# Kernel optimization log

Hardware: AMD Instinct MI355X
Metric: run time of the kernel (lower is better)

The kernel has to match this reference:

```python
import jax, jax.numpy as jnp
import numpy as np

N = 100000   # nodes
E = 800000   # edges (avg degree 8)
IN = 128     # in_dim
H = 128      # hidden_dim
L = 3        # num_layers
EPS = 1e-5   # torch LayerNorm default


def setup_inputs() -> dict:
    key = jax.random.key(0)
    ks = jax.random.split(key, 10)
    s = 0.05
    # DAG edge list: src < dst guarantees acyclicity and node N-1 is a sink.
    rng = np.random.default_rng(0)
    src = rng.integers(0, N - 1, size=E)
    dst = src + 1 + (rng.random(E) * (N - 1 - src)).astype(np.int64)
    return {
        "node_feats": jax.random.normal(ks[0], (N, IN), jnp.float32),
        "src": jnp.asarray(src, jnp.int32),
        "dst": jnp.asarray(dst, jnp.int32),
        "W_in": jax.random.normal(ks[1], (IN, H), jnp.float32) * s,
        "b_in": jnp.zeros((H,), jnp.float32),
        "Ws": jax.random.normal(ks[2], (L, H, H), jnp.float32) * s,
        "bs": jnp.zeros((L, H), jnp.float32),
        "Wn": jax.random.normal(ks[3], (L, H, H), jnp.float32) * s,
        "bn": jnp.zeros((L, H), jnp.float32),
        "Wg": jax.random.normal(ks[4], (L, 2 * H, H), jnp.float32) * s,
        "bg": jnp.zeros((L, H), jnp.float32),
        "gamma": jnp.ones((L, H), jnp.float32),
        "beta": jnp.zeros((L, H), jnp.float32),
        "W_att": jax.random.normal(ks[5], (H, H), jnp.float32) * s,
        "b_att": jnp.zeros((H,), jnp.float32),
        "W_score": jax.random.normal(ks[6], (H, 1), jnp.float32) * s,
        "b_score": jnp.zeros((1,), jnp.float32),
    }


def reference(node_feats, src, dst, W_in, b_in, Ws, bs, Wn, bn, Wg, bg,
              gamma, beta, W_att, b_att, W_score, b_score):
    n = node_feats.shape[0]
    ones_e = jnp.ones(src.shape, node_feats.dtype)
    indeg = jax.ops.segment_sum(ones_e, dst, num_segments=n)          # [N]
    has_pred = (indeg > 0).astype(node_feats.dtype)[:, None]          # [N,1]
    inv_deg = (1.0 / jnp.maximum(indeg, 1.0))[:, None]                # [N,1]
    outdeg = jax.ops.segment_sum(ones_e, src, num_segments=n)
    sink_mask = outdeg == 0                                           # [N]

    h = node_feats @ W_in + b_in                                      # [N,H]
    for i in range(Ws.shape[0]):
        hs = h @ Ws[i] + bs[i]
        # predecessor mean of layer-input h (no within-layer recurrence)
        neigh = jax.ops.segment_sum(h[src], dst, num_segments=n) * inv_deg
        hn = neigh @ Wn[i] + bn[i]
        m = hs + has_pred * hn  # nodes with no preds use m = hs only (bias too)
        gate = jax.nn.sigmoid(jnp.concatenate([h, m], axis=-1) @ Wg[i] + bg[i])
        v = gate * m + (1.0 - gate) * h
        mu = v.mean(-1, keepdims=True)
        var = ((v - mu) ** 2).mean(-1, keepdims=True)
        v = (v - mu) * jax.lax.rsqrt(var + EPS) * gamma[i] + beta[i]
        h = jax.nn.relu(v)

    # attention pooling over sink nodes only
    a = jnp.tanh(h @ W_att + b_att)
    scores = (a @ W_score)[:, 0] + b_score[0]
    scores = jnp.where(sink_mask, scores, -jnp.inf)
    w = jax.nn.softmax(scores, axis=0)  # zero weight on non-sinks
    graph_emb = (w[:, None] * h).sum(0)
    return h, graph_emb
```

## Files before the change

kernel.cpp:

```cpp
#include <hip/hip_runtime.h>
#include <cmath>

typedef unsigned short u16;
typedef unsigned int   u32;
typedef __attribute__((ext_vector_type(8))) short bf16x8;
typedef __attribute__((ext_vector_type(4))) float f32x4;
typedef __attribute__((ext_vector_type(4))) u32   u32x4;

__device__ __forceinline__ float bf2f(u16 u){
    union { u32 i; float f; } x; x.i = ((u32)u) << 16; return x.f;
}
__device__ __forceinline__ u16 f2bf(float f){
    union { float f; u32 i; } x; x.f = f;
    u32 r = x.i + 0x7fffu + ((x.i >> 16) & 1u);
    return (u16)(r >> 16);
}

__device__ __forceinline__ size_t frag_idx(int n, int k){
    int t = n >> 4, sl = n & 15, kk = k >> 5, g16 = (k >> 3) & 3, e = k & 7;
    return ((size_t)(t*4 + kk)*64 + g16*16 + sl)*8 + e;
}


__global__ void k_count(const int* __restrict__ src, const int* __restrict__ dst,
                        int* cnt, int* notsink, int* pos, int E){
    int e = blockIdx.x*256 + threadIdx.x;
    if (e < E){
        pos[e] = atomicAdd(&cnt[dst[e]], 1);
        notsink[src[e]] = 1;
    }
}

__global__ void k_scan1(const int* __restrict__ in, int* blocksum, int N){
    __shared__ int sh[256];
    int tid = threadIdx.x;
    int base = blockIdx.x*1024 + tid*4;
    int s = 0;
    for (int j=0;j<4;j++){ int i = base+j; s += (i < N) ? in[i] : 0; }
    sh[tid] = s; __syncthreads();
    for (int d=128; d>0; d>>=1){ if (tid < d) sh[tid] += sh[tid+d]; __syncthreads(); }
    if (tid == 0) blocksum[blockIdx.x] = sh[0];
}

__global__ void k_scan2(int* blocksum, int nb){
    if (threadIdx.x == 0){
        int run = 0;
        for (int i=0;i<nb;i++){ int v = blocksum[i]; blocksum[i] = run; run += v; }
    }
}

__global__ void k_scan3(const int* __restrict__ in, const int* __restrict__ blockoff,
                        int* out, float* inv_deg, float* haspred, int N){
    __shared__ int sh[256];
    int tid = threadIdx.x;
    int base = blockIdx.x*1024 + tid*4;
    int e[4]; int s = 0;
    for (int j=0;j<4;j++){ int i = base+j; e[j] = (i < N) ? in[i] : 0; s += e[j]; }
    sh[tid] = s; __syncthreads();
    for (int d=1; d<256; d<<=1){
        int t = (tid >= d) ? sh[tid-d] : 0;
        __syncthreads();
        sh[tid] += t;
        __syncthreads();
    }
    int excl = sh[tid] - s + blockoff[blockIdx.x];
    for (int j=0;j<4;j++){
        int i = base+j;
        if (i < N){
            out[i] = excl; excl += e[j];
            inv_deg[i] = 1.0f / (float)(e[j] > 1 ? e[j] : 1);
            haspred[i] = e[j] > 0 ? 1.0f : 0.0f;
        }
    }
}

__global__ void k_place(const int* __restrict__ src, const int* __restrict__ dst,
                        const int* __restrict__ row_ptr, const int* __restrict__ pos,
                        int* csr_src, int E){
    int e = blockIdx.x*256 + threadIdx.x;
    if (e < E)
        csr_src[row_ptr[dst[e]] + pos[e]] = src[e];
}

__global__ void k_wt_plain(const float* __restrict__ W_in, const float* __restrict__ W_att,
                           const float* __restrict__ Ws, const float* __restrict__ Wn,
                           u16* WT_in, u16* WT_att, u16* WB){
    int i = blockIdx.x*256 + threadIdx.x;
    if (i < 32768){
        const float* srcm = (i < 16384) ? W_in : W_att;
        u16* dstm = (i < 16384) ? WT_in : WT_att;
        int w = i & 16383, n = w >> 7, k = w & 127;
        dstm[n*128 + k] = f2bf(srcm[k*128 + n]);
    } else {
        int off = i - 32768;
        int m  = off / 49152;
        int w  = off % 49152;
        int l  = w >> 14, ww = w & 16383;
        int n  = ww >> 7, k = ww & 127;
        const float* srcm = m ? Wn : Ws;
        u16* dstm = WB + ((size_t)l*2 + m)*32768;
        dstm[frag_idx(n, k)] = f2bf(srcm[(size_t)l*16384 + k*128 + n]);
    }
}

__global__ void k_wt_comp(const float* __restrict__ Ws, const float* __restrict__ Wn,
                          const float* __restrict__ Wg,
                          const float* __restrict__ bs, const float* __restrict__ bn,
                          u16* WB, float* vb){
    __shared__ float cols[2][128];
    int l = blockIdx.x / 129;
    int b = blockIdx.x % 129;
    const float* Wgb = Wg + (size_t)l*32768 + 16384;
    int tid = threadIdx.x;
    if (b == 128){
        int n = tid & 127;
        const float* bv = (tid < 128) ? (bs + l*128) : (bn + l*128);
        float acc = 0.f;
        for (int j=0;j<128;j++) acc += bv[j] * Wgb[j*128 + n];
        vb[l*256 + (tid>>7)*128 + n] = acc;
        return;
    }
    int m  = b >> 6;
    int n0 = (b & 63) * 2;
    int nn = tid >> 7, k = tid & 127;
    cols[tid>>7][tid&127] = Wgb[(size_t)(tid&127)*128 + n0 + (tid>>7)];
    __syncthreads();
    const float* A = (m ? Wn : Ws) + (size_t)l*16384;
    float acc = 0.f;
    for (int j=0;j<128;j++) acc += A[k*128 + j] * cols[nn][j];
    int n = n0 + nn;
    if (m == 0) acc += Wg[(size_t)l*32768 + k*128 + n];
    u16* dstm = WB + ((size_t)l*2 + m)*32768;
    dstm[frag_idx(128 + n, k)] = f2bf(acc);
}


__global__ void k_neigh(const u16* __restrict__ h, const int* __restrict__ row_ptr,
                        const int* __restrict__ indeg, const float* __restrict__ inv_deg,
                        const int* __restrict__ csr_src, u16* __restrict__ neigh, int N){
    int wid  = (blockIdx.x*256 + threadIdx.x) >> 6;
    int lane = threadIdx.x & 63;
    int sub = lane >> 4, sl = lane & 15;
    int node = wid*4 + sub;
    bool valid = node < N;
    int deg   = valid ? indeg[node]   : 0;
    int start = valid ? row_ptr[node] : 0;
    float acc[8] = {0.f,0.f,0.f,0.f,0.f,0.f,0.f,0.f};
    for (int e0 = 0; __any(e0 < deg); e0 += 16){
        int idx = 0;
        if (e0 + sl < deg) idx = csr_src[start + e0 + sl];
        int cnt = deg - e0;
        #pragma unroll
        for (int j = 0; j < 16; j++){
            int sidx = __shfl(idx, (sub << 4) | j);
            if (j < cnt){
                bf16x8 v = *(const bf16x8*)(h + (size_t)sidx*128 + sl*8);
                #pragma unroll
                for (int t=0;t<8;t++) acc[t] += bf2f((u16)v[t]);
            }
        }
    }
    if (valid){
        float iv = inv_deg[node];
        u16 o[8];
        #pragma unroll
        for (int t=0;t<8;t++) o[t] = f2bf(acc[t]*iv);
        *(u32x4*)(neigh + (size_t)node*128 + sl*8) = *(const u32x4*)o;
    }
}


__device__ __forceinline__ void stage_A_bf16(const u16* __restrict__ A, u16 (*lA)[136],
                                             int row0, int n_rows, int tid){
    #pragma unroll
    for (int i=0;i<4;i++){
        int c = i*256 + tid;
        int r = c >> 4, col8 = (c & 15) * 8;
        u32x4 v = {0,0,0,0};
        if (row0 + r < n_rows)
            v = *(const u32x4*)(A + (size_t)(row0 + r)*128 + col8);
        *(u32x4*)&lA[r][col8] = v;
    }
}

__device__ __forceinline__ void stage_A_f32(const float* __restrict__ A, u16 (*lA)[136],
                                            int row0, int n_rows, int tid){
    #pragma unroll
    for (int i=0;i<4;i++){
        int c = i*256 + tid;
        int r = c >> 4, col8 = (c & 15) * 8;
        u16 o[8] = {0,0,0,0,0,0,0,0};
        if (row0 + r < n_rows){
            float4 v0 = *(const float4*)(A + (size_t)(row0 + r)*128 + col8);
            float4 v1 = *(const float4*)(A + (size_t)(row0 + r)*128 + col8 + 4);
            o[0]=f2bf(v0.x); o[1]=f2bf(v0.y); o[2]=f2bf(v0.z); o[3]=f2bf(v0.w);
            o[4]=f2bf(v1.x); o[5]=f2bf(v1.y); o[6]=f2bf(v1.z); o[7]=f2bf(v1.w);
        }
        *(u32x4*)&lA[r][col8] = *(const u32x4*)o;
    }
}

__device__ __forceinline__ void stage_B(const u16* __restrict__ BT, int Ks, int koff0,
                                        u16 (*lB)[136], int tid){
    #pragma unroll
    for (int i=0;i<8;i++){
        int c = i*256 + tid;
        int n = c >> 4, col8 = (c & 15) * 8;
        u32x4 v = *(const u32x4*)(BT + (size_t)n*Ks + koff0 + col8);
        *(u32x4*)&lB[n][col8] = v;
    }
}

__device__ __forceinline__ void mfma_tile(const u16 (*lA)[136], const u16 (*lB)[136],
                                          int wave, int lane, f32x4* acc){
    #pragma unroll
    for (int kk=0;kk<4;kk++){
        int koff = kk*32 + (lane >> 4) * 8;
        bf16x8 a = *(const bf16x8*)&lA[wave*16 + (lane & 15)][koff];
        #pragma unroll
        for (int t=0;t<8;t++){
            bf16x8 b = *(const bf16x8*)&lB[t*16 + (lane & 15)][koff];
            acc[t] = __builtin_amdgcn_mfma_f32_16x16x32_bf16(a, b, acc[t], 0, 0, 0);
        }
    }
}


__global__ __launch_bounds__(256) void k_gemm_in(
    const float* __restrict__ A, const u16* __restrict__ BT,
    const float* __restrict__ bias, u16* __restrict__ C, int n_rows)
{
    __shared__ u16 lA[64][136];
    __shared__ u16 lB[128][136];
    int tid = threadIdx.x, wave = tid >> 6, lane = tid & 63;
    int row0 = blockIdx.x * 64;
    f32x4 acc[8];
    #pragma unroll
    for (int t=0;t<8;t++) acc[t] = (f32x4){0.f,0.f,0.f,0.f};
    stage_A_f32(A, lA, row0, n_rows, tid);
    stage_B(BT, 128, 0, lB, tid);
    __syncthreads();
    mfma_tile(lA, lB, wave, lane, acc);

    int sl = lane & 15;
    int rbase = wave*16 + (lane >> 4)*4;
    float bc[8];
    #pragma unroll
    for (int t=0;t<8;t++) bc[t] = bias[t*16 + sl];
    for (int r=0;r<4;r++){
        int row = row0 + rbase + r;
        if (row >= n_rows) continue;
        #pragma unroll
        for (int t=0;t<8;t++)
            C[(size_t)row*128 + t*16 + sl] = f2bf(acc[t][r] + bc[t]);
    }
}


__global__ __launch_bounds__(256, 3) void k_layer(
    const u16* __restrict__ H, const u16* __restrict__ Ng,
    const u16* __restrict__ WB,
    const float* __restrict__ bs, const float* __restrict__ bn,
    const float* __restrict__ bg,
    const float* __restrict__ vb1, const float* __restrict__ vb2,
    const float* __restrict__ gamma, const float* __restrict__ beta,
    const float* __restrict__ haspred,
    u16* __restrict__ Hb, float* __restrict__ Hf, int n_rows)
{
    __shared__ u16 lH[64][132];
    __shared__ u16 lB[2][8192];
    int tid = threadIdx.x, wave = tid >> 6, lane = tid & 63;
    int sl = lane & 15, g16 = lane >> 4;
    int row0 = blockIdx.x * 64;

    int arow = row0 + wave*16 + sl;
    bool av = arow < n_rows;
    bf16x8 a1[4], a2[4];
    #pragma unroll
    for (int kk=0;kk<4;kk++){
        a1[kk] = (bf16x8){0,0,0,0,0,0,0,0};
        a2[kk] = (bf16x8){0,0,0,0,0,0,0,0};
    }
    if (av){
        #pragma unroll
        for (int kk=0;kk<4;kk++){
            a1[kk] = *(const bf16x8*)(H  + (size_t)arow*128 + kk*32 + g16*8);
            a2[kk] = *(const bf16x8*)(Ng + (size_t)arow*128 + kk*32 + g16*8);
        }
    }

    #pragma unroll
    for (int i=0;i<4;i++){
        int c = i*256 + tid;
        int r = c >> 4, col8 = (c & 15) * 8;
        u32x4 v = {0,0,0,0};
        if (row0 + r < n_rows)
            v = *(const u32x4*)(H + (size_t)(row0 + r)*128 + col8);
        *(u32x4*)&lH[r][col8] = v;
    }

    u32x4 st[4];
    #pragma unroll
    for (int i=0;i<4;i++)
        st[i] = *(const u32x4*)(WB + (size_t)(i*256 + tid)*8);
    #pragma unroll
    for (int i=0;i<4;i++)
        *(u32x4*)&lB[0][(i*256 + tid)*8] = st[i];

    f32x4 acc[16];
    #pragma unroll
    for (int t=0;t<16;t++) acc[t] = (f32x4){0.f,0.f,0.f,0.f};
    __syncthreads();

    #pragma unroll
    for (int s=0;s<8;s++){
        int cur = s & 1;
        if (s < 7){
            const u16* sp = WB + (size_t)(s+1)*8192;
            #pragma unroll
            for (int i=0;i<4;i++)
                st[i] = *(const u32x4*)(sp + (size_t)(i*256 + tid)*8);
        }
        const u16* bp = &lB[cur][lane*8];
        #pragma unroll
        for (int j=0;j<4;j++){
            #pragma unroll
            for (int kk=0;kk<4;kk++){
                bf16x8 b = *(const bf16x8*)(bp + ((j*4 + kk) << 9));
                int ai = (s & 3)*4 + j;
                acc[ai] = __builtin_amdgcn_mfma_f32_16x16x32_bf16(
                    (s >= 4) ? a2[kk] : a1[kk], b, acc[ai], 0, 0, 0);
            }
        }
        if (s < 7){
            #pragma unroll
            for (int i=0;i<4;i++)
                *(u32x4*)&lB[cur ^ 1][(i*256 + tid)*8] = st[i];
        }
        __syncthreads();
    }

    int rbase = wave*16 + g16*4;
    float bM[8], bnl[8], bG[8], vb2l[8], gam[8], bet[8];
    #pragma unroll
    for (int t=0;t<8;t++){
        int c = t*16 + sl;
        bM[t] = bs[c]; bnl[t] = bn[c];
        bG[t] = bg[c] + vb1[c]; vb2l[t] = vb2[c];
        gam[t] = gamma[c]; bet[t] = beta[c];
    }
    for (int r=0;r<4;r++){
        int row = row0 + rbase + r;
        if (row >= n_rows) continue;
        float hp = haspred[row];
        float v[8], s = 0.f;
        #pragma unroll
        for (int t=0;t<8;t++){
            int c = t*16 + sl;
            float m = acc[t][r]   + bM[t] + hp*bnl[t];
            float x = acc[t+8][r] + bG[t] + hp*vb2l[t];
            float gg = 1.f/(1.f + expf(-x));
            float hv = bf2f(lH[rbase + r][c]);
            v[t] = gg*m + (1.f - gg)*hv;
            s += v[t];
        }
        s += __shfl_xor(s,1); s += __shfl_xor(s,2); s += __shfl_xor(s,4); s += __shfl_xor(s,8);
        float mu = s * (1.f/128.f);
        float q = 0.f;
        #pragma unroll
        for (int t=0;t<8;t++){ float d = v[t]-mu; q += d*d; }
        q += __shfl_xor(q,1); q += __shfl_xor(q,2); q += __shfl_xor(q,4); q += __shfl_xor(q,8);
        float rs = rsqrtf(q*(1.f/128.f) + 1e-5f);
        #pragma unroll
        for (int t=0;t<8;t++){
            size_t idx = (size_t)row*128 + t*16 + sl;
            float o = (v[t]-mu)*rs*gam[t] + bet[t];
            o = o > 0.f ? o : 0.f;
            Hb[idx] = f2bf(o);
            if (Hf) Hf[idx] = o;
        }
    }
}


__global__ __launch_bounds__(256) void k_gemm_att(
    const u16* __restrict__ H, const u16* __restrict__ BT,
    const float* __restrict__ b_att, const float* __restrict__ Wsc,
    const float* __restrict__ bsc, const int* __restrict__ notsink,
    float* __restrict__ scores, int n_rows)
{
    __shared__ u16 lA[64][136];
    __shared__ u16 lB[128][136];
    int tid = threadIdx.x, wave = tid >> 6, lane = tid & 63;
    int row0 = blockIdx.x * 64;
    f32x4 acc[8];
    #pragma unroll
    for (int t=0;t<8;t++) acc[t] = (f32x4){0.f,0.f,0.f,0.f};
    stage_A_bf16(H, lA, row0, n_rows, tid);
    stage_B(BT, 128, 0, lB, tid);
    __syncthreads();
    mfma_tile(lA, lB, wave, lane, acc);

    int sl = lane & 15;
    int rbase = wave*16 + (lane >> 4)*4;
    float bac[8], wc[8];
    #pragma unroll
    for (int t=0;t<8;t++){ bac[t] = b_att[t*16 + sl]; wc[t] = Wsc[t*16 + sl]; }
    float b0 = bsc[0];
    for (int r=0;r<4;r++){
        int row = row0 + rbase + r;
        if (row >= n_rows) continue;
        float p = 0.f;
        #pragma unroll
        for (int t=0;t<8;t++) p += tanhf(acc[t][r] + bac[t]) * wc[t];
        p += __shfl_xor(p,1); p += __shfl_xor(p,2); p += __shfl_xor(p,4); p += __shfl_xor(p,8);
        if (sl == 0)
            scores[row] = (notsink[row] == 0) ? (p + b0) : -INFINITY;
    }
}


__global__ void k_pool1(const u16* __restrict__ h, const float* __restrict__ scores,
                        float* accum, float* part, int N){
    __shared__ float sh[256];
    __shared__ float sw[256];
    int tid = threadIdx.x;
    int col = tid & 127, grp = tid >> 7;
    float acc = 0.f, wsum = 0.f;
    for (int n = blockIdx.x*2 + grp; n < N; n += 512){
        float s = scores[n];
        if (s > -1e30f){
            float w = expf(s);
            acc += w * bf2f(h[(size_t)n*128 + col]);
            if (col == 0) wsum += w;
        }
    }
    sh[tid] = acc; sw[tid] = wsum; __syncthreads();
    if (tid < 128) sw[tid] += sw[tid+128];
    __syncthreads();
    for (int d=64; d>0; d>>=1){ if (tid < d) sw[tid] += sw[tid+d]; __syncthreads(); }
    if (tid < 128) atomicAdd(&accum[col], sh[tid] + sh[tid+128]);
    if (tid == 0) part[blockIdx.x] = sw[0];
}

__global__ void k_pool2(const float* __restrict__ part, const float* __restrict__ accum,
                        float* __restrict__ out){
    __shared__ float sh[256];
    int tid = threadIdx.x;
    sh[tid] = part[tid]; __syncthreads();
    for (int d=128; d>0; d>>=1){ if (tid < d) sh[tid] += sh[tid+d]; __syncthreads(); }
    if (tid < 128) out[tid] = accum[tid] / sh[0];
}


extern "C" void kernel_launch(void* const* d_in, const int* in_sizes, int n_in,
                              void* d_out, int out_size, void* d_ws, size_t ws_size,
                              hipStream_t stream)
{
    const float* node_feats = (const float*)d_in[0];
    const int* src     = (const int*)d_in[1];
    const int* dst     = (const int*)d_in[2];
    const float* W_in    = (const float*)d_in[3];
    const float* b_in    = (const float*)d_in[4];
    const float* Ws      = (const float*)d_in[5];
    const float* bs      = (const float*)d_in[6];
    const float* Wn      = (const float*)d_in[7];
    const float* bn      = (const float*)d_in[8];
    const float* Wg      = (const float*)d_in[9];
    const float* bg      = (const float*)d_in[10];
    const float* gamma   = (const float*)d_in[11];
    const float* beta    = (const float*)d_in[12];
    const float* W_att   = (const float*)d_in[13];
    const float* b_att   = (const float*)d_in[14];
    const float* W_score = (const float*)d_in[15];
    const float* b_score = (const float*)d_in[16];

    const int N = in_sizes[0] / 128;
    const int E = in_sizes[1];

    char* w = (char*)d_ws;
    auto alloc = [&](size_t bytes)->char* {
        char* p = w; w += (bytes + 255) & ~(size_t)255; return p;
    };
    u16* WT_in  = (u16*)alloc(128*128*2);
    u16* WT_att = (u16*)alloc(128*128*2);
    u16* WB     = (u16*)alloc(3*2*256*128*2);
    float* vb   = (float*)alloc(3*256*4);
    int* cnt      = (int*)alloc((size_t)N*4);
    int* notsink  = (int*)alloc((size_t)N*4);
    float* emb_accum = (float*)alloc(128*4);
    size_t zero_bytes = (size_t)((char*)(emb_accum + 128) - (char*)cnt);
    int* pos      = (int*)alloc((size_t)E*4);
    int* row_ptr  = (int*)alloc((size_t)N*4);
    int* blocksum = (int*)alloc(1024*4);
    int* csr_src  = (int*)alloc((size_t)E*4);
    float* inv_deg = (float*)alloc((size_t)N*4);
    float* haspred = (float*)alloc((size_t)N*4);
    float* scores  = (float*)alloc((size_t)N*4);
    float* part    = (float*)alloc(256*4);
    u16* buf0 = (u16*)alloc((size_t)N*128*2);
    u16* buf1 = (u16*)alloc((size_t)N*128*2);
    u16* bufn = (u16*)alloc((size_t)N*128*2);

    float* h_out   = (float*)d_out;
    float* emb_out = h_out + (size_t)N*128;

    hipMemsetAsync(cnt, 0, zero_bytes, stream);

    k_wt_plain<<<512, 256, 0, stream>>>(W_in, W_att, Ws, Wn, WT_in, WT_att, WB);
    k_wt_comp<<<3*129, 256, 0, stream>>>(Ws, Wn, Wg, bs, bn, WB, vb);

    k_count<<<(E+255)/256, 256, 0, stream>>>(src, dst, cnt, notsink, pos, E);

    int nb = (N + 1023) / 1024;
    k_scan1<<<nb, 256, 0, stream>>>(cnt, blocksum, N);
    k_scan2<<<1, 256, 0, stream>>>(blocksum, nb);
    k_scan3<<<nb, 256, 0, stream>>>(cnt, blocksum, row_ptr, inv_deg, haspred, N);
    k_place<<<(E+255)/256, 256, 0, stream>>>(src, dst, row_ptr, pos, csr_src, E);

    int gblk = (N + 63) / 64;
    int nblk = (N + 15) / 16;

    k_gemm_in<<<gblk, 256, 0, stream>>>(node_feats, WT_in, b_in, buf0, N);

    u16* hin = buf0;
    for (int i=0;i<3;i++){
        k_neigh<<<nblk, 256, 0, stream>>>(hin, row_ptr, cnt, inv_deg, csr_src, bufn, N);
        u16* hb  = (hin == buf0) ? buf1 : buf0;
        float* hf = (i == 2) ? h_out : nullptr;
        k_layer<<<gblk, 256, 0, stream>>>(hin, bufn,
                                          WB + (size_t)i*65536,
                                          bs + i*128, bn + i*128, bg + i*128,
                                          vb + i*256, vb + i*256 + 128,
                                          gamma + i*128, beta + i*128, haspred,
                                          hb, hf, N);
        hin = hb;
    }

    k_gemm_att<<<gblk, 256, 0, stream>>>(hin, WT_att, b_att, W_score, b_score,
                                         notsink, scores, N);
    k_pool1<<<256, 256, 0, stream>>>(hin, scores, emb_accum, part, N);
    k_pool2<<<1, 256, 0, stream>>>(part, emb_accum, emb_out);

    (void)n_in; (void)out_size; (void)ws_size;
}
```

Measured before the change: 600.4 us.

## Restrict attention scoring and pooling to a compacted list of sink nodes

Builds a compacted list of sink nodes right after degree counting, then runs the attention GEMM and tanh scoring only on those rows instead of all N nodes. Pooling becomes a single-block weighted sum over the sink list, which replaces the two-stage atomic reduction. This removes the full-graph attention GEMM and the scan over all scores. The cost is that sink order is nondeterministic (atomic append) and the pool is serialized into one block, which could be slow if sinks were numerous.

```diff
diff --git a/kernel.cpp b/kernel.cpp
--- a/kernel.cpp
+++ b/kernel.cpp
@@ -28,6 +28,15 @@
     if (e < E){
         pos[e] = atomicAdd(&cnt[dst[e]], 1);
         notsink[src[e]] = 1;
+    }
+}
+
+__global__ void k_sinklist(const int* __restrict__ notsink, int* sink_list,
+                           int* nsink, int N){
+    int i = blockIdx.x*256 + threadIdx.x;
+    if (i < N && notsink[i] == 0){
+        int p = atomicAdd(nsink, 1);
+        sink_list[p] = i;
     }
 }
 
@@ -170,19 +179,6 @@
 }
 
 
-__device__ __forceinline__ void stage_A_bf16(const u16* __restrict__ A, u16 (*lA)[136],
-                                             int row0, int n_rows, int tid){
-    #pragma unroll
-    for (int i=0;i<4;i++){
-        int c = i*256 + tid;
-        int r = c >> 4, col8 = (c & 15) * 8;
-        u32x4 v = {0,0,0,0};
-        if (row0 + r < n_rows)
-            v = *(const u32x4*)(A + (size_t)(row0 + r)*128 + col8);
-        *(u32x4*)&lA[r][col8] = v;
-    }
-}
-
 __device__ __forceinline__ void stage_A_f32(const float* __restrict__ A, u16 (*lA)[136],
                                             int row0, int n_rows, int tid){
     #pragma unroll
@@ -383,73 +379,76 @@
 }
 
 
-__global__ __launch_bounds__(256) void k_gemm_att(
+__global__ __launch_bounds__(256) void k_att_sink(
     const u16* __restrict__ H, const u16* __restrict__ BT,
     const float* __restrict__ b_att, const float* __restrict__ Wsc,
-    const float* __restrict__ bsc, const int* __restrict__ notsink,
-    float* __restrict__ scores, int n_rows)
+    const float* __restrict__ bsc, const int* __restrict__ sink_list,
+    const int* __restrict__ nsink, float* __restrict__ scores_sink)
 {
     __shared__ u16 lA[64][136];
     __shared__ u16 lB[128][136];
+    int ns = *nsink;
     int tid = threadIdx.x, wave = tid >> 6, lane = tid & 63;
-    int row0 = blockIdx.x * 64;
-    f32x4 acc[8];
-    #pragma unroll
-    for (int t=0;t<8;t++) acc[t] = (f32x4){0.f,0.f,0.f,0.f};
-    stage_A_bf16(H, lA, row0, n_rows, tid);
+    int sl = lane & 15;
     stage_B(BT, 128, 0, lB, tid);
-    __syncthreads();
-    mfma_tile(lA, lB, wave, lane, acc);
-
-    int sl = lane & 15;
-    int rbase = wave*16 + (lane >> 4)*4;
     float bac[8], wc[8];
     #pragma unroll
     for (int t=0;t<8;t++){ bac[t] = b_att[t*16 + sl]; wc[t] = Wsc[t*16 + sl]; }
     float b0 = bsc[0];
-    for (int r=0;r<4;r++){
-        int row = row0 + rbase + r;
-        if (row >= n_rows) continue;
-        float p = 0.f;
-        #pragma unroll
-        for (int t=0;t<8;t++) p += tanhf(acc[t][r] + bac[t]) * wc[t];
-        p += __shfl_xor(p,1); p += __shfl_xor(p,2); p += __shfl_xor(p,4); p += __shfl_xor(p,8);
-        if (sl == 0)
-            scores[row] = (notsink[row] == 0) ? (p + b0) : -INFINITY;
-    }
-}
-
-
-__global__ void k_pool1(const u16* __restrict__ h, const float* __restrict__ scores,
-                        float* accum, float* part, int N){
+    int rbase = wave*16 + (lane >> 4)*4;
+
+    for (int c0 = blockIdx.x*64; c0 < ns; c0 += gridDim.x*64){
+        __syncthreads();
+        #pragma unroll
+        for (int i=0;i<4;i++){
+            int c = i*256 + tid;
+            int r = c >> 4, col8 = (c & 15) * 8;
+            u32x4 v = {0,0,0,0};
+            if (c0 + r < ns){
+                int row = sink_list[c0 + r];
+                v = *(const u32x4*)(H + (size_t)row*128 + col8);
+            }
+            *(u32x4*)&lA[r][col8] = v;
+        }
+        __syncthreads();
+        f32x4 acc[8];
+        #pragma unroll
+        for (int t=0;t<8;t++) acc[t] = (f32x4){0.f,0.f,0.f,0.f};
+        mfma_tile(lA, lB, wave, lane, acc);
+
+        for (int r=0;r<4;r++){
+            int i = c0 + rbase + r;
+            if (i >= ns) continue;
+            float p = 0.f;
+            #pragma unroll
+            for (int t=0;t<8;t++) p += tanhf(acc[t][r] + bac[t]) * wc[t];
+            p += __shfl_xor(p,1); p += __shfl_xor(p,2); p += __shfl_xor(p,4); p += __shfl_xor(p,8);
+            if (sl == 0)
+                scores_sink[i] = p + b0;
+        }
+    }
+}
+
+
+__global__ void k_pool_sink(const u16* __restrict__ h, const int* __restrict__ sink_list,
+                            const int* __restrict__ nsink,
+                            const float* __restrict__ scores_sink,
+                            float* __restrict__ out){
     __shared__ float sh[256];
-    __shared__ float sw[256];
+    __shared__ float swg[2];
+    int ns = *nsink;
     int tid = threadIdx.x;
     int col = tid & 127, grp = tid >> 7;
     float acc = 0.f, wsum = 0.f;
-    for (int n = blockIdx.x*2 + grp; n < N; n += 512){
-        float s = scores[n];
-        if (s > -1e30f){
-            float w = expf(s);
-            acc += w * bf2f(h[(size_t)n*128 + col]);
-            if (col == 0) wsum += w;
-        }
-    }
-    sh[tid] = acc; sw[tid] = wsum; __syncthreads();
-    if (tid < 128) sw[tid] += sw[tid+128];
+    for (int i = grp; i < ns; i += 2){
+        float w = expf(scores_sink[i]);
+        acc += w * bf2f(h[(size_t)sink_list[i]*128 + col]);
+        if (col == 0) wsum += w;
+    }
+    sh[tid] = acc;
+    if (col == 0) swg[grp] = wsum;
     __syncthreads();
-    for (int d=64; d>0; d>>=1){ if (tid < d) sw[tid] += sw[tid+d]; __syncthreads(); }
-    if (tid < 128) atomicAdd(&accum[col], sh[tid] + sh[tid+128]);
-    if (tid == 0) part[blockIdx.x] = sw[0];
-}
-
-__global__ void k_pool2(const float* __restrict__ part, const float* __restrict__ accum,
-                        float* __restrict__ out){
-    __shared__ float sh[256];
-    int tid = threadIdx.x;
-    sh[tid] = part[tid]; __syncthreads();
-    for (int d=128; d>0; d>>=1){ if (tid < d) sh[tid] += sh[tid+d]; __syncthreads(); }
-    if (tid < 128) out[tid] = accum[tid] / sh[0];
+    if (tid < 128) out[tid] = (sh[tid] + sh[tid+128]) / (swg[0] + swg[1]);
 }
 
 
@@ -488,16 +487,16 @@
     float* vb   = (float*)alloc(3*256*4);
     int* cnt      = (int*)alloc((size_t)N*4);
     int* notsink  = (int*)alloc((size_t)N*4);
-    float* emb_accum = (float*)alloc(128*4);
-    size_t zero_bytes = (size_t)((char*)(emb_accum + 128) - (char*)cnt);
+    int* nsink    = (int*)alloc(256);
+    size_t zero_bytes = (size_t)((char*)nsink + 256 - (char*)cnt);
     int* pos      = (int*)alloc((size_t)E*4);
     int* row_ptr  = (int*)alloc((size_t)N*4);
     int* blocksum = (int*)alloc(1024*4);
     int* csr_src  = (int*)alloc((size_t)E*4);
     float* inv_deg = (float*)alloc((size_t)N*4);
     float* haspred = (float*)alloc((size_t)N*4);
-    float* scores  = (float*)alloc((size_t)N*4);
-    float* part    = (float*)alloc(256*4);
+    int* sink_list = (int*)alloc((size_t)N*4);
+    float* scores_sink = (float*)alloc((size_t)N*4);
     u16* buf0 = (u16*)alloc((size_t)N*128*2);
     u16* buf1 = (u16*)alloc((size_t)N*128*2);
     u16* bufn = (u16*)alloc((size_t)N*128*2);
@@ -511,6 +510,7 @@
     k_wt_comp<<<3*129, 256, 0, stream>>>(Ws, Wn, Wg, bs, bn, WB, vb);
 
     k_count<<<(E+255)/256, 256, 0, stream>>>(src, dst, cnt, notsink, pos, E);
+    k_sinklist<<<(N+255)/256, 256, 0, stream>>>(notsink, sink_list, nsink, N);
 
     int nb = (N + 1023) / 1024;
     k_scan1<<<nb, 256, 0, stream>>>(cnt, blocksum, N);
@@ -537,10 +537,9 @@
         hin = hb;
     }
 
-    k_gemm_att<<<gblk, 256, 0, stream>>>(hin, WT_att, b_att, W_score, b_score,
-                                         notsink, scores, N);
-    k_pool1<<<256, 256, 0, stream>>>(hin, scores, emb_accum, part, N);
-    k_pool2<<<1, 256, 0, stream>>>(part, emb_accum, emb_out);
+    k_att_sink<<<8, 256, 0, stream>>>(hin, WT_att, b_att, W_score, b_score,
+                                      sink_list, nsink, scores_sink);
+    k_pool_sink<<<1, 256, 0, stream>>>(hin, sink_list, nsink, scores_sink, emb_out);
 
     (void)n_in; (void)out_size; (void)ws_size;
 }
```

After: 531.5 us. 1.13x faster.
